# Performance work log

Measured on AMD Instinct MI355X. Metric: run time of the kernel, lower is better.

Reference implementation:

```python
import jax, jax.numpy as jnp
import numpy as np

NLAYER = 3
EPS = 1e-5
NEG = -1e30  # stand-in for -inf in masked max


def _layernorm(h, g, b):
    mu = h.mean(-1, keepdims=True)
    v = ((h - mu) ** 2).mean(-1, keepdims=True)
    return (h - mu) * jax.lax.rsqrt(v + EPS) * g + b


def setup_inputs() -> dict:
    key = jax.random.key(0)
    ks = jax.random.split(key, 8)
    N, K, D = 8192, 8, 128
    s = 0.05
    x = jax.random.normal(ks[0], (N, D), jnp.float32)
    neigh = jax.random.randint(ks[1], (N, K), 0, N, dtype=jnp.int32)
    nbr_count = jax.random.randint(ks[2], (N,), 0, K + 1, dtype=jnp.int32)
    gcn_W = jax.random.normal(ks[3], (NLAYER, D, D), jnp.float32) * s
    gcn_b = jnp.zeros((NLAYER, D), jnp.float32)
    gcn_ln_g = jnp.ones((NLAYER, D), jnp.float32)
    gcn_ln_b = jnp.zeros((NLAYER, D), jnp.float32)
    sage_pool_W = jax.random.normal(ks[4], (D, D), jnp.float32) * s
    sage_pool_b = jnp.zeros((D,), jnp.float32)
    sage_merge_W = jax.random.normal(ks[5], (NLAYER, D, 2 * D), jnp.float32) * s
    sage_merge_b = jnp.zeros((NLAYER, D), jnp.float32)
    sage_ln_g = jnp.ones((NLAYER - 1, D), jnp.float32)
    sage_ln_b = jnp.zeros((NLAYER - 1, D), jnp.float32)
    return {"x": x, "neigh": neigh, "nbr_count": nbr_count,
            "gcn_W": gcn_W, "gcn_b": gcn_b, "gcn_ln_g": gcn_ln_g, "gcn_ln_b": gcn_ln_b,
            "sage_pool_W": sage_pool_W, "sage_pool_b": sage_pool_b,
            "sage_merge_W": sage_merge_W, "sage_merge_b": sage_merge_b,
            "sage_ln_g": sage_ln_g, "sage_ln_b": sage_ln_b}


def reference(x, neigh, nbr_count, gcn_W, gcn_b, gcn_ln_g, gcn_ln_b,
              sage_pool_W, sage_pool_b, sage_merge_W, sage_merge_b,
              sage_ln_g, sage_ln_b):
    N, D = x.shape
    K = neigh.shape[1]
    mask = jnp.arange(K)[None, :] < nbr_count[:, None]  # [N, K] valid neighbors

    # ---- GCN branch: dense symmetric-normalized adjacency with self loops ----
    rows = jnp.broadcast_to(jnp.arange(N)[:, None], neigh.shape)
    A = jnp.zeros((N, N), x.dtype).at[rows, neigh].add(mask.astype(x.dtype))
    A = jnp.minimum(A, 1.0)  # dedupe multi-edges (original sets 1.0)
    A = A.at[jnp.arange(N), jnp.arange(N)].set(1.0)  # self loop (node[0] in list)
    dinv = jax.lax.rsqrt(A.sum(-1))  # degree^-0.5, >= 1 due to self loop
    Ah = dinv[:, None] * A * dinv[None, :]

    h = x
    first = None
    for i in range(NLAYER):
        nxt = h @ gcn_W[i].T + gcn_b[i]
        if i == 0:
            first = nxt
        nxt = jax.nn.relu(Ah @ nxt)
        # residual=True: layer 1 adds first-layer pre-prop enc, later layers add h
        h = _layernorm(nxt + (first if i == 0 else h), gcn_ln_g[i], gcn_ln_b[i])
    gcn_out = h

    # ---- SAGE branch: max-pool over children (self excluded), concat, merge ----
    def pool(node_encs):
        g = jnp.where(mask[:, :, None], node_encs[neigh], NEG)  # [N, K, D]
        p = g.max(axis=1)
        return jnp.where((nbr_count > 0)[:, None], p, 0.0)  # leaf -> zeros

    ne1 = jax.nn.relu(x @ sage_pool_W.T + sage_pool_b)  # pool linear only layer 1
    s = jax.nn.relu(jnp.concatenate([x, pool(ne1)], -1) @ sage_merge_W[0].T + sage_merge_b[0])
    for i in range(1, NLAYER):
        nxt = jax.nn.relu(jnp.concatenate([s, pool(s)], -1) @ sage_merge_W[i].T + sage_merge_b[i])
        s = _layernorm(nxt + s, sage_ln_g[i - 1], sage_ln_b[i - 1])

    return jnp.concatenate([gcn_out, s], -1)  # [N, 2*treehid]
```

## Files before the change

kernel.cpp:

```cpp
#include <hip/hip_runtime.h>

#define NND 8192
#define KNBR 8
#define DD 128
#define EPSF 1e-5f
#define BSTRF 136
#define TILE (128 * BSTRF)

typedef __attribute__((ext_vector_type(8))) short bf16x8;
typedef __attribute__((ext_vector_type(4))) float f32x4;

__device__ __forceinline__ unsigned short f2bf(float f) {
    unsigned u = __float_as_uint(f);
    u += 0x7FFF + ((u >> 16) & 1);
    return (unsigned short)(u >> 16);
}

__device__ __forceinline__ bf16x8 cvt8(const float* __restrict__ p) {
    float4 lo = *(const float4*)p;
    float4 hi = *(const float4*)(p + 4);
    bf16x8 r;
    r[0] = f2bf(lo.x); r[1] = f2bf(lo.y); r[2] = f2bf(lo.z); r[3] = f2bf(lo.w);
    r[4] = f2bf(hi.x); r[5] = f2bf(hi.y); r[6] = f2bf(hi.z); r[7] = f2bf(hi.w);
    return r;
}

__device__ __forceinline__ void stage_cvt(unsigned short* sh, const float* __restrict__ W,
                                          int wstr, int tid) {
    int r = tid >> 1, c = (tid & 1) * 64;
    const float* src = W + (size_t)r * wstr + c;
    unsigned short* d = sh + r * BSTRF + c;
#pragma unroll
    for (int i = 0; i < 8; ++i)
        *(bf16x8*)(d + i * 8) = cvt8(src + i * 8);
}

__device__ __forceinline__ void mma_f32(const float* __restrict__ A, int rowBase,
        const unsigned short* shB, int lane, f32x4* acc) {
    int idx = lane & 15, q = lane >> 4;
    const float* Arow = A + (size_t)(rowBase + idx) * DD;
#pragma unroll
    for (int s = 0; s < 4; ++s) {
        bf16x8 af = cvt8(Arow + s * 32 + q * 8);
#pragma unroll
        for (int ct = 0; ct < 8; ++ct) {
            bf16x8 bf = *(const bf16x8*)(shB + (ct * 16 + idx) * BSTRF + s * 32 + q * 8);
            acc[ct] = __builtin_amdgcn_mfma_f32_16x16x32_bf16(af, bf, acc[ct], 0, 0, 0);
        }
    }
}

__device__ __forceinline__ void mma_bf(const unsigned short* __restrict__ A, int rowBase,
        const unsigned short* shB, int lane, f32x4* acc) {
    int idx = lane & 15, q = lane >> 4;
    const unsigned short* Arow = A + (size_t)(rowBase + idx) * DD;
    bf16x8 af[4];
#pragma unroll
    for (int s = 0; s < 4; ++s) af[s] = *(const bf16x8*)(Arow + s * 32 + q * 8);
#pragma unroll
    for (int s = 0; s < 4; ++s)
#pragma unroll
        for (int ct = 0; ct < 8; ++ct) {
            bf16x8 bf = *(const bf16x8*)(shB + (ct * 16 + idx) * BSTRF + s * 32 + q * 8);
            acc[ct] = __builtin_amdgcn_mfma_f32_16x16x32_bf16(af[s], bf, acc[ct], 0, 0, 0);
        }
}

__device__ __forceinline__ void store_fw(float* __restrict__ out, int ostride, int oOff,
        int rowBase, int lane, const f32x4* acc, const float* __restrict__ bias, bool relu) {
    int idx = lane & 15, q = lane >> 4;
#pragma unroll
    for (int ct = 0; ct < 8; ++ct) {
        float b = bias[ct * 16 + idx];
#pragma unroll
        for (int r = 0; r < 4; ++r) {
            float v = acc[ct][r] + b;
            if (relu) v = fmaxf(v, 0.f);
            out[(size_t)(rowBase + q * 4 + r) * ostride + oOff + ct * 16 + idx] = v;
        }
    }
}

__device__ __forceinline__ void store_fw_b16(unsigned short* __restrict__ out,
        int rowBase, int lane, const f32x4* acc, const float* __restrict__ bias) {
    int idx = lane & 15, q = lane >> 4;
#pragma unroll
    for (int ct = 0; ct < 8; ++ct) {
        float b = bias[ct * 16 + idx];
#pragma unroll
        for (int r = 0; r < 4; ++r)
            out[(size_t)(rowBase + q * 4 + r) * DD + ct * 16 + idx]
                = f2bf(fmaxf(acc[ct][r] + b, 0.f));
    }
}

__device__ __forceinline__ void lnstore_fw(float* __restrict__ out, int ostride, int oOff,
        const float* __restrict__ resid, int rowBase, int lane, f32x4* acc,
        const float* __restrict__ bias, const float* __restrict__ g,
        const float* __restrict__ bv, unsigned short* __restrict__ outB) {
    int idx = lane & 15, q = lane >> 4;
    float rsum[4] = {0.f, 0.f, 0.f, 0.f};
#pragma unroll
    for (int ct = 0; ct < 8; ++ct) {
        float b = bias[ct * 16 + idx];
#pragma unroll
        for (int r = 0; r < 4; ++r) {
            float t = fmaxf(acc[ct][r] + b, 0.f)
                    + resid[(size_t)(rowBase + q * 4 + r) * DD + ct * 16 + idx];
            acc[ct][r] = t;
            rsum[r] += t;
        }
    }
#pragma unroll
    for (int r = 0; r < 4; ++r)
#pragma unroll
        for (int m = 1; m < 16; m <<= 1) rsum[r] += __shfl_xor(rsum[r], m, 64);
    float mu[4];
#pragma unroll
    for (int r = 0; r < 4; ++r) mu[r] = rsum[r] * (1.f / 128.f);
    float var[4] = {0.f, 0.f, 0.f, 0.f};
#pragma unroll
    for (int ct = 0; ct < 8; ++ct)
#pragma unroll
        for (int r = 0; r < 4; ++r) {
            float d = acc[ct][r] - mu[r];
            var[r] += d * d;
        }
#pragma unroll
    for (int r = 0; r < 4; ++r)
#pragma unroll
        for (int m = 1; m < 16; m <<= 1) var[r] += __shfl_xor(var[r], m, 64);
    float rs[4];
#pragma unroll
    for (int r = 0; r < 4; ++r) rs[r] = rsqrtf(var[r] * (1.f / 128.f) + EPSF);
#pragma unroll
    for (int ct = 0; ct < 8; ++ct) {
        float gg = g[ct * 16 + idx], bb = bv[ct * 16 + idx];
#pragma unroll
        for (int r = 0; r < 4; ++r) {
            float o = (acc[ct][r] - mu[r]) * rs[r] * gg + bb;
            size_t row = (size_t)(rowBase + q * 4 + r);
            out[row * ostride + oOff + ct * 16 + idx] = o;
            if (outB) outB[row * DD + ct * 16 + idx] = f2bf(o);
        }
    }
}

__global__ __launch_bounds__(256)
void mega_gemm(const float* __restrict__ x,
               const float* __restrict__ gcnW, const float* __restrict__ poolW,
               const float* __restrict__ mW,
               const float* __restrict__ gB0, const float* __restrict__ pB,
               const float* __restrict__ mB0,
               const int* __restrict__ neigh, const int* __restrict__ cnt,
               float* __restrict__ dinv, int* __restrict__ kept,
               float* __restrict__ G, unsigned short* __restrict__ E1b,
               float* __restrict__ S) {
    __shared__ unsigned short shB[TILE];
    const int tid = threadIdx.x;
    const int grp = blockIdx.y;
    const float* W; int wstr;
    if (grp == 0)      { W = gcnW;  wstr = 128; }
    else if (grp == 1) { W = poolW; wstr = 128; }
    else               { W = mW;    wstr = 256; }
    stage_cvt(shB, W, wstr, tid);
    __syncthreads();
    const int lane = tid & 63, w = tid >> 6;
    const int rowBase = ((int)blockIdx.x * 4 + w) * 16;
    f32x4 acc[8];
#pragma unroll
    for (int i = 0; i < 8; ++i) acc[i] = (f32x4){0.f, 0.f, 0.f, 0.f};
    mma_f32(x, rowBase, shB, lane, acc);
    if (grp == 0)      store_fw(G, DD, 0, rowBase, lane, acc, gB0, false);
    else if (grp == 1) store_fw_b16(E1b, rowBase, lane, acc, pB);
    else               store_fw(S, DD, 0, rowBase, lane, acc, mB0, false);

    if (grp == 0 && blockIdx.x < 32) {
        int i = (int)blockIdx.x * 256 + tid;
        int c = cnt[i];
        int nb[KNBR];
#pragma unroll
        for (int j = 0; j < KNBR; ++j) nb[j] = neigh[i * KNBR + j];
        int mask = 0, deg = 1;
#pragma unroll
        for (int j = 0; j < KNBR; ++j) {
            if (j < c) {
                int v = nb[j];
                bool dup = (v == i);
                for (int jj = 0; jj < j; ++jj)
                    if (nb[jj] == v) { dup = true; }
                if (!dup) { mask |= (1 << j); deg++; }
            }
        }
        dinv[i] = rsqrtf((float)deg);
        kept[i] = mask;
    }
}

__global__ __launch_bounds__(256)
void gemm_step4(const unsigned short* __restrict__ Pb, const unsigned short* __restrict__ H1b,
                const float* __restrict__ mW, const float* __restrict__ gcnW,
                const float* __restrict__ gB1,
                float* __restrict__ S, unsigned short* __restrict__ S1b,
                float* __restrict__ G) {
    __shared__ unsigned short shB[TILE];
    const int tid = threadIdx.x;
    const int lane = tid & 63, w = tid >> 6;
    const int rowBase = ((int)blockIdx.x * 4 + w) * 16;
    f32x4 acc[8];
#pragma unroll
    for (int i = 0; i < 8; ++i) acc[i] = (f32x4){0.f, 0.f, 0.f, 0.f};
    if (blockIdx.y == 0) {
        stage_cvt(shB, mW + 128, 256, tid);
        __syncthreads();
        mma_bf(Pb, rowBase, shB, lane, acc);
        int idx = lane & 15, q = lane >> 4;
#pragma unroll
        for (int ct = 0; ct < 8; ++ct)
#pragma unroll
            for (int r = 0; r < 4; ++r) {
                size_t o = (size_t)(rowBase + q * 4 + r) * DD + ct * 16 + idx;
                float v = fmaxf(S[o] + acc[ct][r], 0.f);
                S[o] = v;
                S1b[o] = f2bf(v);
            }
    } else {
        stage_cvt(shB, gcnW + 16384, 128, tid);
        __syncthreads();
        mma_bf(H1b, rowBase, shB, lane, acc);
        store_fw(G, DD, 0, rowBase, lane, acc, gB1, false);
    }
}

__global__ __launch_bounds__(256)
void gemm_step6(const unsigned short* __restrict__ S1b, const unsigned short* __restrict__ Pb,
                const unsigned short* __restrict__ H2b, const float* __restrict__ S1,
                const float* __restrict__ mW, const float* __restrict__ gcnW,
                const float* __restrict__ mB1, const float* __restrict__ gB2,
                const float* __restrict__ sg, const float* __restrict__ sb,
                float* __restrict__ S2, unsigned short* __restrict__ S2b,
                float* __restrict__ G) {
    __shared__ unsigned short shB[2 * TILE];
    const int tid = threadIdx.x;
    const int lane = tid & 63, w = tid >> 6;
    const int rowBase = ((int)blockIdx.x * 4 + w) * 16;
    f32x4 acc[8];
#pragma unroll
    for (int i = 0; i < 8; ++i) acc[i] = (f32x4){0.f, 0.f, 0.f, 0.f};
    if (blockIdx.y == 0) {
        stage_cvt(shB, mW + 32768, 256, tid);
        stage_cvt(shB + TILE, mW + 32768 + 128, 256, tid);
        __syncthreads();
        mma_bf(S1b, rowBase, shB, lane, acc);
        mma_bf(Pb, rowBase, shB + TILE, lane, acc);
        lnstore_fw(S2, DD, 0, S1, rowBase, lane, acc, mB1, sg, sb, S2b);
    } else {
        stage_cvt(shB, gcnW + 32768, 128, tid);
        __syncthreads();
        mma_bf(H2b, rowBase, shB, lane, acc);
        store_fw(G, DD, 0, rowBase, lane, acc, gB2, false);
    }
}

__global__ __launch_bounds__(256)
void gemm_final(const unsigned short* __restrict__ S2b, const unsigned short* __restrict__ Pb,
                const float* __restrict__ S2,
                const float* __restrict__ mW, const float* __restrict__ mB2,
                const float* __restrict__ sg2, const float* __restrict__ sb2,
                float* __restrict__ out) {
    __shared__ unsigned short shB[2 * TILE];
    const int tid = threadIdx.x;
    const int lane = tid & 63, w = tid >> 6;
    const int rowBase = ((int)blockIdx.x * 4 + w) * 16;
    f32x4 acc[8];
#pragma unroll
    for (int i = 0; i < 8; ++i) acc[i] = (f32x4){0.f, 0.f, 0.f, 0.f};
    stage_cvt(shB, mW + 65536, 256, tid);
    stage_cvt(shB + TILE, mW + 65536 + 128, 256, tid);
    __syncthreads();
    mma_bf(S2b, rowBase, shB, lane, acc);
    mma_bf(Pb, rowBase, shB + TILE, lane, acc);
    lnstore_fw(out, 2 * DD, DD, S2, rowBase, lane, acc, mB2, sg2, sb2, nullptr);
}

__device__ __forceinline__ float wave_sum(float s) {
#pragma unroll
    for (int m = 1; m < 64; m <<= 1) s += __shfl_xor(s, m, 64);
    return s;
}

__device__ __forceinline__ void prop_ln_row(int row, int lane,
        const float* __restrict__ nxt, const float* __restrict__ resid,
        const float* __restrict__ dinv, const int* __restrict__ kept,
        const int* __restrict__ neigh,
        const float* __restrict__ g, const float* __restrict__ b,
        float* __restrict__ out, int oStride, int oOff,
        unsigned short* __restrict__ outB) {
    const float2* nxt2 = (const float2*)nxt;
    float di = dinv[row];
    int km = kept[row];
    int idxs[KNBR]; float wj[KNBR];
#pragma unroll
    for (int j = 0; j < KNBR; ++j) {
        int nb = neigh[row * KNBR + j];
        bool k = (km >> j) & 1;
        idxs[j] = k ? nb : row;
        wj[j] = k ? dinv[nb] : 0.f;
    }
    float2 vv[KNBR];
#pragma unroll
    for (int j = 0; j < KNBR; ++j) vv[j] = nxt2[(size_t)idxs[j] * 64 + lane];
    float2 self = nxt2[(size_t)row * 64 + lane];
    float ax = di * self.x, ay = di * self.y;
#pragma unroll
    for (int j = 0; j < KNBR; ++j) {
        ax = fmaf(wj[j], vv[j].x, ax);
        ay = fmaf(wj[j], vv[j].y, ay);
    }
    float2 r = ((const float2*)resid)[(size_t)row * 64 + lane];
    float vx = fmaxf(di * ax, 0.f) + r.x;
    float vy = fmaxf(di * ay, 0.f) + r.y;
    float mu = wave_sum(vx + vy) * (1.f / 128.f);
    float dx = vx - mu, dy = vy - mu;
    float var = wave_sum(dx * dx + dy * dy) * (1.f / 128.f);
    float rs = rsqrtf(var + EPSF);
    float2 gg = ((const float2*)g)[lane];
    float2 bb = ((const float2*)b)[lane];
    float2 o;
    o.x = dx * rs * gg.x + bb.x;
    o.y = dy * rs * gg.y + bb.y;
    *reinterpret_cast<float2*>(out + (size_t)row * oStride + oOff + lane * 2) = o;
    if (outB) {
        unsigned pk = (unsigned)f2bf(o.x) | ((unsigned)f2bf(o.y) << 16);
        *(unsigned*)(outB + (size_t)row * DD + lane * 2) = pk;
    }
}

__device__ __forceinline__ void pool_row_b(int row, int lane,
        const unsigned short* __restrict__ enc, const int* __restrict__ neigh,
        const int* __restrict__ cnt, unsigned short* __restrict__ P) {
    int c = cnt[row];
    const unsigned* e32 = (const unsigned*)enc;
    unsigned vv[KNBR];
#pragma unroll
    for (int j = 0; j < KNBR; ++j) {
        int nb = neigh[row * KNBR + j];
        int src = (j < c) ? nb : row;
        vv[j] = e32[(size_t)src * 64 + lane];
    }
    float ax = -1e30f, ay = -1e30f;
#pragma unroll
    for (int j = 0; j < KNBR; ++j) {
        if (j < c) {
            ax = fmaxf(ax, __uint_as_float(vv[j] << 16));
            ay = fmaxf(ay, __uint_as_float(vv[j] & 0xFFFF0000u));
        }
    }
    unsigned o = 0u;
    if (c > 0)
        o = (__float_as_uint(ax) >> 16) | (__float_as_uint(ay) & 0xFFFF0000u);
    ((unsigned*)P)[(size_t)row * 64 + lane] = o;
}

__global__ __launch_bounds__(256)
void prop_pool_kernel(const float* __restrict__ nxt, const float* __restrict__ resid,
                      const float* __restrict__ dinv, const int* __restrict__ kept,
                      const int* __restrict__ neigh, const int* __restrict__ cnt,
                      const float* __restrict__ g, const float* __restrict__ b,
                      float* __restrict__ outH, int oStride, int oOff,
                      unsigned short* __restrict__ outHB,
                      const unsigned short* __restrict__ enc,
                      unsigned short* __restrict__ P) {
    int row = blockIdx.x * 4 + (threadIdx.x >> 6);
    int lane = threadIdx.x & 63;
    prop_ln_row(row, lane, nxt, resid, dinv, kept, neigh, g, b, outH, oStride, oOff, outHB);
    pool_row_b(row, lane, enc, neigh, cnt, P);
}

extern "C" void kernel_launch(void* const* d_in, const int* in_sizes, int n_in,
                              void* d_out, int out_size, void* d_ws, size_t ws_size,
                              hipStream_t stream) {
    (void)in_sizes; (void)n_in; (void)out_size; (void)ws_size;
    const float* x      = (const float*)d_in[0];
    const int*   neigh  = (const int*)d_in[1];
    const int*   cnt    = (const int*)d_in[2];
    const float* gcnW   = (const float*)d_in[3];
    const float* gcnB   = (const float*)d_in[4];
    const float* gcnG   = (const float*)d_in[5];
    const float* gcnBb  = (const float*)d_in[6];
    const float* poolW  = (const float*)d_in[7];
    const float* poolB  = (const float*)d_in[8];
    const float* mW     = (const float*)d_in[9];
    const float* mB     = (const float*)d_in[10];
    const float* sg     = (const float*)d_in[11];
    const float* sb     = (const float*)d_in[12];
    float* out = (float*)d_out;

    char* ws = (char*)d_ws;
    float* dinv = (float*)ws;
    int*   kept = (int*)(ws + 32 * 1024);
    float* G  = (float*)(ws + 64 * 1024);
    float* H1 = G  + NND * DD;
    float* H2 = H1 + NND * DD;
    float* S1 = H2 + NND * DD;
    float* S2 = S1 + NND * DD;
    unsigned short* E1b = (unsigned short*)(S2 + NND * DD);
    unsigned short* Pb  = E1b + NND * DD;
    unsigned short* H1b = Pb  + NND * DD;
    unsigned short* H2b = H1b + NND * DD;
    unsigned short* S1b = H2b + NND * DD;
    unsigned short* S2b = S1b + NND * DD;

    dim3 blk(256);
    dim3 rgrid(NND / 4);

    mega_gemm<<<dim3(128, 3), blk, 0, stream>>>(x, gcnW, poolW, mW, gcnB, poolB, mB,
                                                neigh, cnt, dinv, kept, G, E1b, S1);
    prop_pool_kernel<<<rgrid, blk, 0, stream>>>(G, G, dinv, kept, neigh, cnt,
                                                gcnG, gcnBb, H1, DD, 0, H1b, E1b, Pb);
    gemm_step4<<<dim3(128, 2), blk, 0, stream>>>(Pb, H1b, mW, gcnW, gcnB + DD,
                                                 S1, S1b, G);
    prop_pool_kernel<<<rgrid, blk, 0, stream>>>(G, H1, dinv, kept, neigh, cnt,
                                                gcnG + DD, gcnBb + DD, H2, DD, 0,
                                                H2b, S1b, Pb);
    gemm_step6<<<dim3(128, 2), blk, 0, stream>>>(S1b, Pb, H2b, S1, mW, gcnW,
                                                 mB + DD, gcnB + 2 * DD, sg, sb,
                                                 S2, S2b, G);
    prop_pool_kernel<<<rgrid, blk, 0, stream>>>(G, H2, dinv, kept, neigh, cnt,
                                                gcnG + 2 * DD, gcnBb + 2 * DD,
                                                out, 2 * DD, 0, nullptr, S2b, Pb);
    gemm_final<<<dim3(128), blk, 0, stream>>>(S2b, Pb, S2, mW, mB + 2 * DD,
                                              sg + DD, sb + DD, out);
}
```

Measured before the change: 152.0 us.

## Pre-convert weights to swizzled bf16 once and stage via global_load_lds

Adds a cvt_deg kernel that converts all weight matrices to bf16 once into a workspace buffer in an XOR-swizzled layout, alongside the degree computation. Each GEMM kernel then copies its tile straight into LDS with global_load_lds instead of converting fp32 weights per block, and loads A fragments before the barrier so the two overlap. gemm_final now splits the two K-halves across wave pairs on twice as many blocks and combines them through an LDS exchange. The cost is one extra kernel launch and extra LDS for the exchange buffer.

```diff
diff --git a/kernel.cpp b/kernel.cpp
--- a/kernel.cpp
+++ b/kernel.cpp
@@ -4,8 +4,8 @@
 #define KNBR 8
 #define DD 128
 #define EPSF 1e-5f
-#define BSTRF 136
-#define TILE (128 * BSTRF)
+#define TSH 16384
+#define XSTR 132
 
 typedef __attribute__((ext_vector_type(8))) short bf16x8;
 typedef __attribute__((ext_vector_type(4))) float f32x4;
@@ -25,43 +25,47 @@
     return r;
 }
 
-__device__ __forceinline__ void stage_cvt(unsigned short* sh, const float* __restrict__ W,
-                                          int wstr, int tid) {
-    int r = tid >> 1, c = (tid & 1) * 64;
-    const float* src = W + (size_t)r * wstr + c;
-    unsigned short* d = sh + r * BSTRF + c;
-#pragma unroll
-    for (int i = 0; i < 8; ++i)
-        *(bf16x8*)(d + i * 8) = cvt8(src + i * 8);
-}
-
-__device__ __forceinline__ void mma_f32(const float* __restrict__ A, int rowBase,
-        const unsigned short* shB, int lane, f32x4* acc) {
-    int idx = lane & 15, q = lane >> 4;
-    const float* Arow = A + (size_t)(rowBase + idx) * DD;
-#pragma unroll
-    for (int s = 0; s < 4; ++s) {
-        bf16x8 af = cvt8(Arow + s * 32 + q * 8);
+__device__ __forceinline__ void gload_lds16(const unsigned short* g, unsigned short* l) {
+    __builtin_amdgcn_global_load_lds(
+        (const __attribute__((address_space(1))) unsigned int*)(g),
+        (__attribute__((address_space(3))) unsigned int*)(l), 16, 0, 0);
+}
+
+template<int NT>
+__device__ __forceinline__ void stageN(unsigned short* sh, const unsigned short* wb, int tid) {
+    int lane = tid & 63, w = tid >> 6;
+#pragma unroll
+    for (int r = 0; r < NT * 8; ++r) {
+        int blk = (r * 4 + w) * 512;
+        gload_lds16(wb + blk + lane * 8, sh + blk);
+    }
+}
+
+__device__ __forceinline__ void load_af(bf16x8* af, const unsigned short* __restrict__ A,
+                                        int rowBase, int lane) {
+    int idx = lane & 15, q = lane >> 4;
+    const unsigned short* Ar = A + (size_t)(rowBase + idx) * DD;
+#pragma unroll
+    for (int s = 0; s < 4; ++s) af[s] = *(const bf16x8*)(Ar + s * 32 + q * 8);
+}
+
+__device__ __forceinline__ void load_af_f32(bf16x8* af, const float* __restrict__ A,
+                                            int rowBase, int lane) {
+    int idx = lane & 15, q = lane >> 4;
+    const float* Ar = A + (size_t)(rowBase + idx) * DD;
+#pragma unroll
+    for (int s = 0; s < 4; ++s) af[s] = cvt8(Ar + s * 32 + q * 8);
+}
+
+__device__ __forceinline__ void mma_sw(const bf16x8* af, const unsigned short* shB,
+                                       int lane, f32x4* acc) {
+    int idx = lane & 15, q = lane >> 4, k7 = idx & 7;
+#pragma unroll
+    for (int s = 0; s < 4; ++s)
 #pragma unroll
         for (int ct = 0; ct < 8; ++ct) {
-            bf16x8 bf = *(const bf16x8*)(shB + (ct * 16 + idx) * BSTRF + s * 32 + q * 8);
-            acc[ct] = __builtin_amdgcn_mfma_f32_16x16x32_bf16(af, bf, acc[ct], 0, 0, 0);
-        }
-    }
-}
-
-__device__ __forceinline__ void mma_bf(const unsigned short* __restrict__ A, int rowBase,
-        const unsigned short* shB, int lane, f32x4* acc) {
-    int idx = lane & 15, q = lane >> 4;
-    const unsigned short* Arow = A + (size_t)(rowBase + idx) * DD;
-    bf16x8 af[4];
-#pragma unroll
-    for (int s = 0; s < 4; ++s) af[s] = *(const bf16x8*)(Arow + s * 32 + q * 8);
-#pragma unroll
-    for (int s = 0; s < 4; ++s)
-#pragma unroll
-        for (int ct = 0; ct < 8; ++ct) {
-            bf16x8 bf = *(const bf16x8*)(shB + (ct * 16 + idx) * BSTRF + s * 32 + q * 8);
+            int ch = (4 * s + q) ^ k7;
+            bf16x8 bf = *(const bf16x8*)(shB + (ct * 16 + idx) * 128 + ch * 8);
             acc[ct] = __builtin_amdgcn_mfma_f32_16x16x32_bf16(af[s], bf, acc[ct], 0, 0, 0);
         }
 }
@@ -147,36 +151,14 @@
 }
 
 __global__ __launch_bounds__(256)
-void mega_gemm(const float* __restrict__ x,
-               const float* __restrict__ gcnW, const float* __restrict__ poolW,
-               const float* __restrict__ mW,
-               const float* __restrict__ gB0, const float* __restrict__ pB,
-               const float* __restrict__ mB0,
-               const int* __restrict__ neigh, const int* __restrict__ cnt,
-               float* __restrict__ dinv, int* __restrict__ kept,
-               float* __restrict__ G, unsigned short* __restrict__ E1b,
-               float* __restrict__ S) {
-    __shared__ unsigned short shB[TILE];
-    const int tid = threadIdx.x;
-    const int grp = blockIdx.y;
-    const float* W; int wstr;
-    if (grp == 0)      { W = gcnW;  wstr = 128; }
-    else if (grp == 1) { W = poolW; wstr = 128; }
-    else               { W = mW;    wstr = 256; }
-    stage_cvt(shB, W, wstr, tid);
-    __syncthreads();
-    const int lane = tid & 63, w = tid >> 6;
-    const int rowBase = ((int)blockIdx.x * 4 + w) * 16;
-    f32x4 acc[8];
-#pragma unroll
-    for (int i = 0; i < 8; ++i) acc[i] = (f32x4){0.f, 0.f, 0.f, 0.f};
-    mma_f32(x, rowBase, shB, lane, acc);
-    if (grp == 0)      store_fw(G, DD, 0, rowBase, lane, acc, gB0, false);
-    else if (grp == 1) store_fw_b16(E1b, rowBase, lane, acc, pB);
-    else               store_fw(S, DD, 0, rowBase, lane, acc, mB0, false);
-
-    if (grp == 0 && blockIdx.x < 32) {
-        int i = (int)blockIdx.x * 256 + tid;
+void cvt_deg(const int* __restrict__ neigh, const int* __restrict__ cnt,
+             const float* __restrict__ gcnW, const float* __restrict__ poolW,
+             const float* __restrict__ mW,
+             float* __restrict__ dinv, int* __restrict__ kept,
+             unsigned short* __restrict__ wbuf) {
+    int bx = blockIdx.x, tid = threadIdx.x;
+    if (bx < 32) {
+        int i = bx * 256 + tid;
         int c = cnt[i];
         int nb[KNBR];
 #pragma unroll
@@ -194,26 +176,59 @@
         }
         dinv[i] = rsqrtf((float)deg);
         kept[i] = mask;
-    }
+    } else {
+        int cid = (bx - 32) * 256 + tid;
+        int t = cid >> 11, c2 = cid & 2047, row = c2 >> 4, ch = c2 & 15;
+        const float* base; int str;
+        if (t < 3)       { base = gcnW + t * 16384; str = 128; }
+        else if (t == 3) { base = poolW; str = 128; }
+        else { int u = t - 4; base = mW + (u >> 1) * 32768 + (u & 1) * 128; str = 256; }
+        bf16x8 v = cvt8(base + (size_t)row * str + ch * 8);
+        *(bf16x8*)(wbuf + t * TSH + row * 128 + ((ch ^ (row & 7)) << 3)) = v;
+    }
+}
+
+__global__ __launch_bounds__(256)
+void mega_gemm(const float* __restrict__ x, const unsigned short* __restrict__ wbuf,
+               const float* __restrict__ gB0, const float* __restrict__ pB,
+               const float* __restrict__ mB0,
+               float* __restrict__ G, unsigned short* __restrict__ E1b,
+               float* __restrict__ S) {
+    __shared__ __align__(16) unsigned short shB[TSH];
+    const int tid = threadIdx.x, lane = tid & 63, w = tid >> 6;
+    const int grp = blockIdx.y;
+    const int tile = (grp == 0) ? 0 : (grp == 1) ? 3 : 4;
+    stageN<1>(shB, wbuf + tile * TSH, tid);
+    const int rowBase = ((int)blockIdx.x * 4 + w) * 16;
+    bf16x8 af[4];
+    load_af_f32(af, x, rowBase, lane);
+    __syncthreads();
+    f32x4 acc[8];
+#pragma unroll
+    for (int i = 0; i < 8; ++i) acc[i] = (f32x4){0.f, 0.f, 0.f, 0.f};
+    mma_sw(af, shB, lane, acc);
+    if (grp == 0)      store_fw(G, DD, 0, rowBase, lane, acc, gB0, false);
+    else if (grp == 1) store_fw_b16(E1b, rowBase, lane, acc, pB);
+    else               store_fw(S, DD, 0, rowBase, lane, acc, mB0, false);
 }
 
 __global__ __launch_bounds__(256)
 void gemm_step4(const unsigned short* __restrict__ Pb, const unsigned short* __restrict__ H1b,
-                const float* __restrict__ mW, const float* __restrict__ gcnW,
-                const float* __restrict__ gB1,
+                const unsigned short* __restrict__ wbuf, const float* __restrict__ gB1,
                 float* __restrict__ S, unsigned short* __restrict__ S1b,
                 float* __restrict__ G) {
-    __shared__ unsigned short shB[TILE];
-    const int tid = threadIdx.x;
-    const int lane = tid & 63, w = tid >> 6;
+    __shared__ __align__(16) unsigned short shB[TSH];
+    const int tid = threadIdx.x, lane = tid & 63, w = tid >> 6;
     const int rowBase = ((int)blockIdx.x * 4 + w) * 16;
     f32x4 acc[8];
 #pragma unroll
     for (int i = 0; i < 8; ++i) acc[i] = (f32x4){0.f, 0.f, 0.f, 0.f};
+    bf16x8 af[4];
     if (blockIdx.y == 0) {
-        stage_cvt(shB, mW + 128, 256, tid);
+        stageN<1>(shB, wbuf + 5 * TSH, tid);
+        load_af(af, Pb, rowBase, lane);
         __syncthreads();
-        mma_bf(Pb, rowBase, shB, lane, acc);
+        mma_sw(af, shB, lane, acc);
         int idx = lane & 15, q = lane >> 4;
 #pragma unroll
         for (int ct = 0; ct < 8; ++ct)
@@ -225,9 +240,10 @@
                 S1b[o] = f2bf(v);
             }
     } else {
-        stage_cvt(shB, gcnW + 16384, 128, tid);
+        stageN<1>(shB, wbuf + 1 * TSH, tid);
+        load_af(af, H1b, rowBase, lane);
         __syncthreads();
-        mma_bf(H1b, rowBase, shB, lane, acc);
+        mma_sw(af, shB, lane, acc);
         store_fw(G, DD, 0, rowBase, lane, acc, gB1, false);
     }
 }
@@ -235,52 +251,72 @@
 __global__ __launch_bounds__(256)
 void gemm_step6(const unsigned short* __restrict__ S1b, const unsigned short* __restrict__ Pb,
                 const unsigned short* __restrict__ H2b, const float* __restrict__ S1,
-                const float* __restrict__ mW, const float* __restrict__ gcnW,
+                const unsigned short* __restrict__ wbuf,
                 const float* __restrict__ mB1, const float* __restrict__ gB2,
                 const float* __restrict__ sg, const float* __restrict__ sb,
                 float* __restrict__ S2, unsigned short* __restrict__ S2b,
                 float* __restrict__ G) {
-    __shared__ unsigned short shB[2 * TILE];
-    const int tid = threadIdx.x;
-    const int lane = tid & 63, w = tid >> 6;
+    __shared__ __align__(16) unsigned short shB[2 * TSH];
+    const int tid = threadIdx.x, lane = tid & 63, w = tid >> 6;
     const int rowBase = ((int)blockIdx.x * 4 + w) * 16;
     f32x4 acc[8];
 #pragma unroll
     for (int i = 0; i < 8; ++i) acc[i] = (f32x4){0.f, 0.f, 0.f, 0.f};
     if (blockIdx.y == 0) {
-        stage_cvt(shB, mW + 32768, 256, tid);
-        stage_cvt(shB + TILE, mW + 32768 + 128, 256, tid);
+        stageN<2>(shB, wbuf + 6 * TSH, tid);
+        bf16x8 af1[4], af2[4];
+        load_af(af1, S1b, rowBase, lane);
+        load_af(af2, Pb, rowBase, lane);
         __syncthreads();
-        mma_bf(S1b, rowBase, shB, lane, acc);
-        mma_bf(Pb, rowBase, shB + TILE, lane, acc);
+        mma_sw(af1, shB, lane, acc);
+        mma_sw(af2, shB + TSH, lane, acc);
         lnstore_fw(S2, DD, 0, S1, rowBase, lane, acc, mB1, sg, sb, S2b);
     } else {
-        stage_cvt(shB, gcnW + 32768, 128, tid);
+        stageN<1>(shB, wbuf + 2 * TSH, tid);
+        bf16x8 af[4];
+        load_af(af, H2b, rowBase, lane);
         __syncthreads();
-        mma_bf(H2b, rowBase, shB, lane, acc);
+        mma_sw(af, shB, lane, acc);
         store_fw(G, DD, 0, rowBase, lane, acc, gB2, false);
     }
 }
 
 __global__ __launch_bounds__(256)
 void gemm_final(const unsigned short* __restrict__ S2b, const unsigned short* __restrict__ Pb,
-                const float* __restrict__ S2,
-                const float* __restrict__ mW, const float* __restrict__ mB2,
+                const float* __restrict__ S2, const unsigned short* __restrict__ wbuf,
+                const float* __restrict__ mB2,
                 const float* __restrict__ sg2, const float* __restrict__ sb2,
                 float* __restrict__ out) {
-    __shared__ unsigned short shB[2 * TILE];
-    const int tid = threadIdx.x;
-    const int lane = tid & 63, w = tid >> 6;
-    const int rowBase = ((int)blockIdx.x * 4 + w) * 16;
+    __shared__ __align__(16) unsigned short shB[2 * TSH];
+    __shared__ float xch[32 * XSTR];
+    const int tid = threadIdx.x, lane = tid & 63, w = tid >> 6;
+    stageN<2>(shB, wbuf + 8 * TSH, tid);
+    const int rowBase = (int)blockIdx.x * 32 + (w & 1) * 16;
+    const int unit = w >> 1;
+    bf16x8 af[4];
+    load_af(af, unit ? Pb : S2b, rowBase, lane);
+    __syncthreads();
     f32x4 acc[8];
 #pragma unroll
     for (int i = 0; i < 8; ++i) acc[i] = (f32x4){0.f, 0.f, 0.f, 0.f};
-    stage_cvt(shB, mW + 65536, 256, tid);
-    stage_cvt(shB + TILE, mW + 65536 + 128, 256, tid);
+    mma_sw(af, shB + unit * TSH, lane, acc);
+    int idx = lane & 15, q = lane >> 4;
+    if (unit) {
+#pragma unroll
+        for (int ct = 0; ct < 8; ++ct)
+#pragma unroll
+            for (int r = 0; r < 4; ++r)
+                xch[((w & 1) * 16 + q * 4 + r) * XSTR + ct * 16 + idx] = acc[ct][r];
+    }
     __syncthreads();
-    mma_bf(S2b, rowBase, shB, lane, acc);
-    mma_bf(Pb, rowBase, shB + TILE, lane, acc);
-    lnstore_fw(out, 2 * DD, DD, S2, rowBase, lane, acc, mB2, sg2, sb2, nullptr);
+    if (!unit) {
+#pragma unroll
+        for (int ct = 0; ct < 8; ++ct)
+#pragma unroll
+            for (int r = 0; r < 4; ++r)
+                acc[ct][r] += xch[((w & 1) * 16 + q * 4 + r) * XSTR + ct * 16 + idx];
+        lnstore_fw(out, 2 * DD, DD, S2, rowBase, lane, acc, mB2, sg2, sb2, nullptr);
+    }
 }
 
 __device__ __forceinline__ float wave_sum(float s) {
@@ -399,7 +435,8 @@
     char* ws = (char*)d_ws;
     float* dinv = (float*)ws;
     int*   kept = (int*)(ws + 32 * 1024);
-    float* G  = (float*)(ws + 64 * 1024);
+    unsigned short* wbuf = (unsigned short*)(ws + 64 * 1024);
+    float* G  = (float*)(ws + 448 * 1024);
     float* H1 = G  + NND * DD;
     float* H2 = H1 + NND * DD;
     float* S1 = H2 + NND * DD;
@@ -414,21 +451,22 @@
     dim3 blk(256);
     dim3 rgrid(NND / 4);
 
-    mega_gemm<<<dim3(128, 3), blk, 0, stream>>>(x, gcnW, poolW, mW, gcnB, poolB, mB,
-                                                neigh, cnt, dinv, kept, G, E1b, S1);
+    cvt_deg<<<dim3(112), blk, 0, stream>>>(neigh, cnt, gcnW, poolW, mW,
+                                           dinv, kept, wbuf);
+    mega_gemm<<<dim3(128, 3), blk, 0, stream>>>(x, wbuf, gcnB, poolB, mB, G, E1b, S1);
     prop_pool_kernel<<<rgrid, blk, 0, stream>>>(G, G, dinv, kept, neigh, cnt,
                                                 gcnG, gcnBb, H1, DD, 0, H1b, E1b, Pb);
-    gemm_step4<<<dim3(128, 2), blk, 0, stream>>>(Pb, H1b, mW, gcnW, gcnB + DD,
+    gemm_step4<<<dim3(128, 2), blk, 0, stream>>>(Pb, H1b, wbuf, gcnB + DD,
                                                  S1, S1b, G);
     prop_pool_kernel<<<rgrid, blk, 0, stream>>>(G, H1, dinv, kept, neigh, cnt,
                                                 gcnG + DD, gcnBb + DD, H2, DD, 0,
                                                 H2b, S1b, Pb);
-    gemm_step6<<<dim3(128, 2), blk, 0, stream>>>(S1b, Pb, H2b, S1, mW, gcnW,
+    gemm_step6<<<dim3(128, 2), blk, 0, stream>>>(S1b, Pb, H2b, S1, wbuf,
                                                  mB + DD, gcnB + 2 * DD, sg, sb,
                                                  S2, S2b, G);
     prop_pool_kernel<<<rgrid, blk, 0, stream>>>(G, H2, dinv, kept, neigh, cnt,
                                                 gcnG + 2 * DD, gcnBb + 2 * DD,
                                                 out, 2 * DD, 0, nullptr, S2b, Pb);
-    gemm_final<<<dim3(128), blk, 0, stream>>>(S2b, Pb, S2, mW, mB + 2 * DD,
+    gemm_final<<<dim3(256), blk, 0, stream>>>(S2b, Pb, S2, wbuf, mB + 2 * DD,
                                               sg + DD, sb + DD, out);
 }
```

Result: faster. 146.0 us (-4.0%).
